# Optimization experiments

Hardware: AMD Instinct MI355X
Metric: run time of the kernel (lower is better)

Reference implementation:

```python
import jax, jax.numpy as jnp
import numpy as np

V, E, H = 50000, 128, 256  # vocab, embedding_size, hidden_size
S, B = 512, 64             # seq_len, batch (seq-first, torch LSTM default)


def setup_inputs() -> dict:
    key = jax.random.key(0)
    ks = jax.random.split(key, 10)
    u = 1.0 / np.sqrt(H)  # torch LSTM/Linear init bound

    def unif(k, sh):
        return jax.random.uniform(k, sh, jnp.float32, -u, u)

    emb = jax.random.normal(ks[0], (V, E), jnp.float32) * 0.02
    emb = emb.at[0].set(0.0)  # padding_idx=0

    inp = {
        "seq": jax.random.randint(ks[1], (S, B), 0, V),
        "emb": emb,
        # forward direction weights (gate order i,f,g,o like torch)
        "W_ih_f": unif(ks[2], (4 * H, E)),
        "W_hh_f": unif(ks[3], (4 * H, H)),
        "b_f": unif(ks[4], (4 * H,)),  # b_ih + b_hh fused (identical math)
        # reverse direction
        "W_ih_b": unif(ks[5], (4 * H, E)),
        "W_hh_b": unif(ks[6], (4 * H, H)),
        "b_b": unif(ks[7], (4 * H,)),
        # classification head over concatenated bi-directional features
        "W_out": unif(ks[8], (1, 2 * H)),
        "b_out": unif(ks[9], (1,)),
    }
    return inp


def _lstm_scan(xg, W_hh):
    """xg: [S,B,4H] precomputed input-gate projections; returns hidden seq [S,B,H]."""
    b = xg.shape[1]
    h0 = jnp.zeros((b, H), xg.dtype)
    c0 = jnp.zeros((b, H), xg.dtype)

    def step(carry, xg_t):
        h, c = carry
        gates = xg_t + h @ W_hh.T  # [B,4H]
        i, f, g, o = jnp.split(gates, 4, axis=-1)
        i = jax.nn.sigmoid(i)
        f = jax.nn.sigmoid(f)
        g = jnp.tanh(g)
        o = jax.nn.sigmoid(o)
        c = f * c + i * g
        h = o * jnp.tanh(c)
        return (h, c), h

    _, hs = jax.lax.scan(step, (h0, c0), xg)
    return hs


def reference(seq, emb, W_ih_f, W_hh_f, b_f, W_ih_b, W_hh_b, b_b, W_out, b_out):
    # embedding with padding_idx=0 (row 0 contributes zero)
    x = jnp.where((seq == 0)[..., None], 0.0, emb[seq])  # [S,B,E]

    xg_f = jnp.einsum("sbe,ge->sbg", x, W_ih_f) + b_f          # [S,B,4H]
    hs_f = _lstm_scan(xg_f, W_hh_f)                             # [S,B,H]

    xr = x[::-1]
    xg_b = jnp.einsum("sbe,ge->sbg", xr, W_ih_b) + b_b
    hs_b = _lstm_scan(xg_b, W_hh_b)[::-1]                       # [S,B,H]

    out = jnp.concatenate([hs_f, hs_b], axis=-1)                # [S,B,2H]
    last = out[-1]                                              # [B,2H]
    return jax.nn.sigmoid(last @ W_out.T + b_out)               # [B,1]
```

## Files before the change

### kernel.cpp

```cpp
#include <hip/hip_runtime.h>
#include <hip/hip_bf16.h>
#include <stdint.h>
#include <string.h>

#define S_LEN 512
#define NBATCH 64
#define EDIM 128
#define HDIM 256
#define GDIM 1024

#define WQ_SCALE 1024.0f
#define HQ_SCALE 127.0f
#define DEQ_SCALE (1.0f / 130048.0f)

typedef __attribute__((ext_vector_type(8))) short short8;
typedef __attribute__((ext_vector_type(4))) short short4v;
typedef __attribute__((ext_vector_type(4))) float float4v;
typedef __attribute__((ext_vector_type(4))) int int4v;

#define OFF_WHH8 0u
#define SZ_WHH8 (256u * 64u * 16u)
#define OFF_WIH (OFF_WHH8 + SZ_WHH8)
#define SZ_WIH (64u * 4u * 64u * 16u)
#define OFF_XG ((size_t)(OFF_WIH + SZ_WIH))
#define SZ_XG ((size_t)S_LEN * NBATCH * GDIM * 2)
#define OFF_HF (OFF_XG + SZ_XG)

__device__ __forceinline__ short f2bf(float f) {
    union { float f; unsigned u; } v;
    v.f = f;
    unsigned r = (v.u + 0x7fffu + ((v.u >> 16) & 1u)) >> 16;
    return (short)r;
}
__device__ __forceinline__ float bf2f(short s) {
    union { unsigned u; float f; } v;
    v.u = ((unsigned)(unsigned short)s) << 16;
    return v.f;
}
__device__ __forceinline__ float sigm(float x) {
    float e = __expf(-x);
    return __builtin_amdgcn_rcpf(1.0f + e);
}
__device__ __forceinline__ float tanh_(float x) {
    float e = __expf(2.0f * x);
    return 1.0f - 2.0f * __builtin_amdgcn_rcpf(e + 1.0f);
}

__global__ __launch_bounds__(256) void prep_frags(const float* __restrict__ src,
                                                  char* __restrict__ dst,
                                                  int K, int nchunks, int nfrags) {
    int id = blockIdx.x * blockDim.x + threadIdx.x;
    int lane = id & 63;
    int f = id >> 6;
    if (f >= nfrags) return;
    int tile = f / nchunks;
    int c = f - tile * nchunks;
    int row = tile * 16 + (lane & 15);
    int k0 = c * 32 + ((lane >> 4) * 8);
    const float* s = src + (size_t)row * K + k0;
    short8 pack;
#pragma unroll
    for (int j = 0; j < 8; ++j) pack[j] = f2bf(s[j]);
    *(short8*)(dst + ((size_t)f * 64 + lane) * 16) = pack;
}

__global__ __launch_bounds__(256) void prep_whh_i8(const float* __restrict__ src,
                                                   char* __restrict__ dst) {
    int id = blockIdx.x * blockDim.x + threadIdx.x;
    int lane = id & 63;
    int f = id >> 6;
    int tile = f >> 2, kc = f & 3;
    int row = tile * 16 + (lane & 15);
    int k0 = kc * 64 + ((lane >> 4) * 16);
    const float* s = src + (size_t)row * HDIM + k0;
    union { char b[16]; int4v v; } u;
#pragma unroll
    for (int b = 0; b < 16; ++b)
        u.b[b] = (char)(int)rintf(s[b] * WQ_SCALE);
    *(int4v*)(dst + ((size_t)f * 64 + lane) * 16) = u.v;
}

__global__ __launch_bounds__(256) void input_proj(const int* __restrict__ seq,
                                                  const float* __restrict__ emb,
                                                  const char* __restrict__ wih_frags,
                                                  const float* __restrict__ bias,
                                                  char* __restrict__ xg) {
    __shared__ __align__(16) short lx[4][16][136];
    int tid = threadIdx.x;
    int t0 = blockIdx.x * 4;
    int g = blockIdx.y;

    {
        int row = tid >> 2;
        int tt = row >> 4, m = row & 15;
        int k0 = (tid & 3) * 32;
        int v = seq[(t0 + tt) * NBATCH + g * 16 + m];
        const float* src = emb + (size_t)v * EDIM + k0;
        bool zero = (v == 0);
#pragma unroll
        for (int u = 0; u < 32; u += 4) {
            float4v f = *(const float4v*)(src + u);
            short4v p;
#pragma unroll
            for (int e = 0; e < 4; ++e) p[e] = zero ? (short)0 : f2bf(f[e]);
            *(short4v*)&lx[tt][m][k0 + u] = p;
        }
    }
    __syncthreads();

    int lane = tid & 63, w = tid >> 6;
    int ln = lane & 15, q = lane >> 4;

    short8 Bx[4][4];
#pragma unroll
    for (int tt = 0; tt < 4; ++tt)
#pragma unroll
        for (int c = 0; c < 4; ++c)
            Bx[tt][c] = *(const short8*)&lx[tt][ln][c * 32 + q * 8];

    for (int nt = 0; nt < 16; ++nt) {
        int tile = w * 16 + nt;
        short8 Aw[4];
#pragma unroll
        for (int c = 0; c < 4; ++c)
            Aw[c] = *(const short8*)(wih_frags + (((size_t)tile * 4 + c) * 64 + lane) * 16);
        float4v b4 = *(const float4v*)(bias + tile * 16 + q * 4);
#pragma unroll
        for (int tt = 0; tt < 4; ++tt) {
            float4v acc = b4;
#pragma unroll
            for (int c = 0; c < 4; ++c)
                acc = __builtin_amdgcn_mfma_f32_16x16x32_bf16(Aw[c], Bx[tt][c], acc, 0, 0, 0);
            short4v p;
#pragma unroll
            for (int r = 0; r < 4; ++r) p[r] = f2bf(acc[r]);
            size_t off = ((size_t)(t0 + tt) * NBATCH + g * 16 + ln) * GDIM + tile * 16 + q * 4;
            *(short4v*)(xg + off * 2) = p;
        }
    }
}

__global__ __launch_bounds__(1024, 4) void lstm_scan(const char* __restrict__ whh8,
                                                     const char* __restrict__ xg,
                                                     float* __restrict__ hf_out) {
    __shared__ __align__(16) char hls[2][16][272];
    __shared__ __align__(16) int scr[16][16 * 20];
    int tid = threadIdx.x;
    int lane = tid & 63, w = tid >> 6;
    int ln = lane & 15, q = lane >> 4;
    int bg = blockIdx.x;

    int4v Wfr[4][4];
#pragma unroll
    for (int blk = 0; blk < 4; ++blk) {
        int tile = 16 * blk + w;
#pragma unroll
        for (int kc = 0; kc < 4; ++kc)
            Wfr[blk][kc] = *(const int4v*)(whh8 + (((size_t)(tile * 4 + kc)) * 64 + lane) * 16);
    }

    {
        int* hp = (int*)&hls[0][0][0];
        for (int i = tid; i < (2 * 16 * 272) / 4; i += 1024) hp[i] = 0;
    }

    const char* hrd = &hls[0][0][0];
    char* hwr = &hls[1][0][0];
    int hoff_rd = ln * 272 + q * 16;

    int b = ln & 3;
    int rr = ln >> 2;
    int j = w * 16 + q * 4 + rr;
    int hoff_wr = b * 272 + j;
    int* swr = &scr[w][0] + (q * 4 + ln) * 20;
    const int* srd = &scr[w][0] + (q * 4 + b) * 20 + rr;

    float cst = 0.0f;

    const char* xgp = xg + (((size_t)(bg * 4 + b) * GDIM + j) * 2);
    const size_t tstep = (size_t)NBATCH * GDIM * 2;

    unsigned short xq[4];
#pragma unroll
    for (int blk = 0; blk < 4; ++blk)
        xq[blk] = *(const unsigned short*)(xgp + blk * 512);

    __syncthreads();

    for (int t = 0; t < S_LEN; ++t) {
        int4v Bh[4];
#pragma unroll
        for (int kc = 0; kc < 4; ++kc)
            Bh[kc] = *(const int4v*)(hrd + hoff_rd + kc * 64);

        float xgf[4];
#pragma unroll
        for (int blk = 0; blk < 4; ++blk) xgf[blk] = bf2f((short)xq[blk]);
        xgp += tstep;
        if (t != S_LEN - 1) {
#pragma unroll
            for (int blk = 0; blk < 4; ++blk)
                xq[blk] = *(const unsigned short*)(xgp + blk * 512);
        }

        int4v a[4];
#pragma unroll
        for (int blk = 0; blk < 4; ++blk) a[blk] = (int4v){0, 0, 0, 0};
#pragma unroll
        for (int kc = 0; kc < 4; ++kc)
#pragma unroll
            for (int blk = 0; blk < 4; ++blk)
                a[blk] = __builtin_amdgcn_mfma_i32_16x16x64_i8(Wfr[blk][kc], Bh[kc], a[blk], 0, 0, 0);

        if (ln < 4) {
#pragma unroll
            for (int blk = 0; blk < 4; ++blk)
                *(int4v*)(swr + blk * 4) = a[blk];
        }
        float gi = fmaf((float)srd[0], DEQ_SCALE, xgf[0]);
        float gf = fmaf((float)srd[4], DEQ_SCALE, xgf[1]);
        float gg = fmaf((float)srd[8], DEQ_SCALE, xgf[2]);
        float go = fmaf((float)srd[12], DEQ_SCALE, xgf[3]);

        float iv = sigm(gi);
        float fv = sigm(gf);
        float gv = tanh_(gg);
        float ov = sigm(go);
        float cv = fv * cst + iv * gv;
        cst = cv;
        float hv = ov * tanh_(cv);

        int hq = (int)rintf(hv * HQ_SCALE);
        hwr[hoff_wr] = (char)hq;

        if (t == S_LEN - 1)
            hf_out[((size_t)(bg * 4 + b)) * HDIM + j] = hv;

        const char* tr = hrd; hrd = hwr; hwr = (char*)tr;
        __syncthreads();
    }
}

__global__ __launch_bounds__(256) void tail_kernel(const int* __restrict__ seq,
                                                   const float* __restrict__ emb,
                                                   const float* __restrict__ wih_b,
                                                   const float* __restrict__ b_b,
                                                   const float* __restrict__ wout,
                                                   const float* __restrict__ b_out,
                                                   const float* __restrict__ hf,
                                                   float* __restrict__ out) {
    __shared__ float xs[EDIM];
    __shared__ float red[4];
    int b = blockIdx.x, tid = threadIdx.x;
    if (tid < EDIM) {
        int v = seq[(S_LEN - 1) * NBATCH + b];
        xs[tid] = (v == 0) ? 0.0f : emb[(size_t)v * EDIM + tid];
    }
    __syncthreads();

    int j = tid;
    float si = b_b[j], sg = b_b[2 * HDIM + j], so = b_b[3 * HDIM + j];
    const float* wi = wih_b + (size_t)j * EDIM;
    const float* wg = wih_b + (size_t)(2 * HDIM + j) * EDIM;
    const float* wo = wih_b + (size_t)(3 * HDIM + j) * EDIM;
#pragma unroll 8
    for (int k = 0; k < EDIM; k += 4) {
        float4v x4 = *(const float4v*)&xs[k];
        float4v a = *(const float4v*)(wi + k);
        float4v c = *(const float4v*)(wg + k);
        float4v d = *(const float4v*)(wo + k);
#pragma unroll
        for (int e = 0; e < 4; ++e) {
            si += a[e] * x4[e];
            sg += c[e] * x4[e];
            so += d[e] * x4[e];
        }
    }
    float cc = sigm(si) * tanh_(sg);
    float hb = sigm(so) * tanh_(cc);
    float partial = hf[(size_t)b * HDIM + j] * wout[j] + hb * wout[HDIM + j];

    float val = partial;
#pragma unroll
    for (int off = 32; off > 0; off >>= 1) val += __shfl_down(val, off, 64);
    int lane = tid & 63, wv = tid >> 6;
    if (lane == 0) red[wv] = val;
    __syncthreads();
    if (tid == 0) out[b] = sigm(red[0] + red[1] + red[2] + red[3] + b_out[0]);
}

extern "C" void kernel_launch(void* const* d_in, const int* in_sizes, int n_in,
                              void* d_out, int out_size, void* d_ws, size_t ws_size,
                              hipStream_t stream) {
    const int* seq = (const int*)d_in[0];
    const float* emb = (const float*)d_in[1];
    const float* Wih_f = (const float*)d_in[2];
    const float* Whh_f = (const float*)d_in[3];
    const float* b_f = (const float*)d_in[4];
    const float* Wih_b = (const float*)d_in[5];
    const float* b_b = (const float*)d_in[7];
    const float* Wout = (const float*)d_in[8];
    const float* b_out = (const float*)d_in[9];
    float* out = (float*)d_out;
    char* ws = (char*)d_ws;

    prep_whh_i8<<<dim3(64), 256, 0, stream>>>(Whh_f, ws + OFF_WHH8);
    prep_frags<<<dim3(64), 256, 0, stream>>>(Wih_f, ws + OFF_WIH, EDIM, 4, 64 * 4);
    input_proj<<<dim3(S_LEN / 4, 4), 256, 0, stream>>>(seq, emb, ws + OFF_WIH, b_f, ws + OFF_XG);
    lstm_scan<<<dim3(16), 1024, 0, stream>>>(ws + OFF_WHH8, ws + OFF_XG, (float*)(ws + OFF_HF));
    tail_kernel<<<dim3(NBATCH), 256, 0, stream>>>(seq, emb, Wih_b, b_b, Wout, b_out,
                                                  (const float*)(ws + OFF_HF), out);
}
```

Measured before the change: 697.6 us.

## Split LSTM scan into 32 blocks of 512 threads with prescaled exp2 gates

The recurrent scan now runs 32 workgroups of 8 waves, each handling 2 batch columns instead of 4, with each wave computing two tiles per gate. This spreads the serial scan across more CUs and shortens the per-step barrier. Gate pre-activations are prescaled in the input projection by -log2e or 2·log2e, and the dequant scale is folded into those constants. Sigmoid and tanh then become a single exp2 plus a fast reciprocal, with slight accuracy risk from bf16 storage of scaled values and approximate rcp.

```diff
diff --git a/kernel.cpp b/kernel.cpp
--- a/kernel.cpp
+++ b/kernel.cpp
@@ -11,7 +11,9 @@
 
 #define WQ_SCALE 1024.0f
 #define HQ_SCALE 127.0f
-#define DEQ_SCALE (1.0f / 130048.0f)
+#define LOG2E 1.4426950408889634f
+#define C_IFO (-1.1093545e-05f)
+#define C_G (2.2187090e-05f)
 
 typedef __attribute__((ext_vector_type(8))) short short8;
 typedef __attribute__((ext_vector_type(4))) short short4v;
@@ -120,6 +122,7 @@
 
     for (int nt = 0; nt < 16; ++nt) {
         int tile = w * 16 + nt;
+        float kg = ((tile >> 4) == 2) ? (2.0f * LOG2E) : (-LOG2E);
         short8 Aw[4];
 #pragma unroll
         for (int c = 0; c < 4; ++c)
@@ -133,60 +136,65 @@
                 acc = __builtin_amdgcn_mfma_f32_16x16x32_bf16(Aw[c], Bx[tt][c], acc, 0, 0, 0);
             short4v p;
 #pragma unroll
-            for (int r = 0; r < 4; ++r) p[r] = f2bf(acc[r]);
+            for (int r = 0; r < 4; ++r) p[r] = f2bf(acc[r] * kg);
             size_t off = ((size_t)(t0 + tt) * NBATCH + g * 16 + ln) * GDIM + tile * 16 + q * 4;
             *(short4v*)(xg + off * 2) = p;
         }
     }
 }
 
-__global__ __launch_bounds__(1024, 4) void lstm_scan(const char* __restrict__ whh8,
-                                                     const char* __restrict__ xg,
-                                                     float* __restrict__ hf_out) {
+__global__ __launch_bounds__(512, 2) void lstm_scan(const char* __restrict__ whh8,
+                                                    const char* __restrict__ xg,
+                                                    float* __restrict__ hf_out) {
     __shared__ __align__(16) char hls[2][16][272];
-    __shared__ __align__(16) int scr[16][16 * 20];
+    __shared__ __align__(16) int scr[8][256];
     int tid = threadIdx.x;
     int lane = tid & 63, w = tid >> 6;
     int ln = lane & 15, q = lane >> 4;
     int bg = blockIdx.x;
 
-    int4v Wfr[4][4];
-#pragma unroll
-    for (int blk = 0; blk < 4; ++blk) {
-        int tile = 16 * blk + w;
-#pragma unroll
-        for (int kc = 0; kc < 4; ++kc)
-            Wfr[blk][kc] = *(const int4v*)(whh8 + (((size_t)(tile * 4 + kc)) * 64 + lane) * 16);
-    }
+    int4v Wfr[4][2][4];
+#pragma unroll
+    for (int g = 0; g < 4; ++g)
+#pragma unroll
+        for (int p = 0; p < 2; ++p) {
+            int tile = g * 16 + (w * 2 + p);
+#pragma unroll
+            for (int kc = 0; kc < 4; ++kc)
+                Wfr[g][p][kc] = *(const int4v*)(whh8 + (((size_t)(tile * 4 + kc)) * 64 + lane) * 16);
+        }
 
     {
         int* hp = (int*)&hls[0][0][0];
-        for (int i = tid; i < (2 * 16 * 272) / 4; i += 1024) hp[i] = 0;
+        for (int i = tid; i < (2 * 16 * 272) / 4; i += 512) hp[i] = 0;
     }
 
     const char* hrd = &hls[0][0][0];
     char* hwr = &hls[1][0][0];
     int hoff_rd = ln * 272 + q * 16;
 
-    int b = ln & 3;
-    int rr = ln >> 2;
-    int j = w * 16 + q * 4 + rr;
+    int b = ln & 1;
+    int rr = (ln >> 1) & 3;
+    int p = ln >> 3;
+    int j = (w * 2 + p) * 16 + q * 4 + rr;
     int hoff_wr = b * 272 + j;
-    int* swr = &scr[w][0] + (q * 4 + ln) * 20;
-    const int* srd = &scr[w][0] + (q * 4 + b) * 20 + rr;
+
+    int* swr = &scr[w][0];
+    const int* srd = &scr[w][0] + (q * 16 + p * 8 + b * 4 + rr);
 
     float cst = 0.0f;
 
-    const char* xgp = xg + (((size_t)(bg * 4 + b) * GDIM + j) * 2);
+    const char* xgp = xg + (((size_t)(bg * 2 + b) * GDIM + j) * 2);
     const size_t tstep = (size_t)NBATCH * GDIM * 2;
 
     unsigned short xq[4];
 #pragma unroll
-    for (int blk = 0; blk < 4; ++blk)
-        xq[blk] = *(const unsigned short*)(xgp + blk * 512);
+    for (int g = 0; g < 4; ++g)
+        xq[g] = *(const unsigned short*)(xgp + g * 512);
 
     __syncthreads();
 
+    const int4v z4 = {0, 0, 0, 0};
     for (int t = 0; t < S_LEN; ++t) {
         int4v Bh[4];
 #pragma unroll
@@ -195,46 +203,54 @@
 
         float xgf[4];
 #pragma unroll
-        for (int blk = 0; blk < 4; ++blk) xgf[blk] = bf2f((short)xq[blk]);
+        for (int g = 0; g < 4; ++g) xgf[g] = bf2f((short)xq[g]);
         xgp += tstep;
         if (t != S_LEN - 1) {
 #pragma unroll
-            for (int blk = 0; blk < 4; ++blk)
-                xq[blk] = *(const unsigned short*)(xgp + blk * 512);
-        }
-
-        int4v a[4];
-#pragma unroll
-        for (int blk = 0; blk < 4; ++blk) a[blk] = (int4v){0, 0, 0, 0};
-#pragma unroll
-        for (int kc = 0; kc < 4; ++kc)
-#pragma unroll
-            for (int blk = 0; blk < 4; ++blk)
-                a[blk] = __builtin_amdgcn_mfma_i32_16x16x64_i8(Wfr[blk][kc], Bh[kc], a[blk], 0, 0, 0);
-
-        if (ln < 4) {
-#pragma unroll
-            for (int blk = 0; blk < 4; ++blk)
-                *(int4v*)(swr + blk * 4) = a[blk];
-        }
-        float gi = fmaf((float)srd[0], DEQ_SCALE, xgf[0]);
-        float gf = fmaf((float)srd[4], DEQ_SCALE, xgf[1]);
-        float gg = fmaf((float)srd[8], DEQ_SCALE, xgf[2]);
-        float go = fmaf((float)srd[12], DEQ_SCALE, xgf[3]);
-
-        float iv = sigm(gi);
-        float fv = sigm(gf);
-        float gv = tanh_(gg);
-        float ov = sigm(go);
-        float cv = fv * cst + iv * gv;
+            for (int g = 0; g < 4; ++g)
+                xq[g] = *(const unsigned short*)(xgp + g * 512);
+        }
+
+        int4v a[4][2];
+#pragma unroll
+        for (int g = 0; g < 4; ++g)
+#pragma unroll
+            for (int pp = 0; pp < 2; ++pp)
+                a[g][pp] = __builtin_amdgcn_mfma_i32_16x16x64_i8(Wfr[g][pp][0], Bh[0], z4, 0, 0, 0);
+#pragma unroll
+        for (int kc = 1; kc < 4; ++kc)
+#pragma unroll
+            for (int g = 0; g < 4; ++g)
+#pragma unroll
+                for (int pp = 0; pp < 2; ++pp)
+                    a[g][pp] = __builtin_amdgcn_mfma_i32_16x16x64_i8(Wfr[g][pp][kc], Bh[kc], a[g][pp], 0, 0, 0);
+
+        if (ln < 2) {
+#pragma unroll
+            for (int g = 0; g < 4; ++g)
+#pragma unroll
+                for (int pp = 0; pp < 2; ++pp)
+                    *(int4v*)(swr + g * 64 + q * 16 + pp * 8 + ln * 4) = a[g][pp];
+        }
+        float s0 = fmaf((float)srd[0], C_IFO, xgf[0]);
+        float s1 = fmaf((float)srd[64], C_IFO, xgf[1]);
+        float s2 = fmaf((float)srd[128], C_G, xgf[2]);
+        float s3 = fmaf((float)srd[192], C_IFO, xgf[3]);
+
+        float iv = __builtin_amdgcn_rcpf(1.0f + exp2f(s0));
+        float fv = __builtin_amdgcn_rcpf(1.0f + exp2f(s1));
+        float gv = fmaf(-2.0f, __builtin_amdgcn_rcpf(1.0f + exp2f(s2)), 1.0f);
+        float ov = __builtin_amdgcn_rcpf(1.0f + exp2f(s3));
+        float cv = fmaf(fv, cst, iv * gv);
         cst = cv;
-        float hv = ov * tanh_(cv);
+        float tc = fmaf(-2.0f, __builtin_amdgcn_rcpf(1.0f + exp2f(cv * (2.0f * LOG2E))), 1.0f);
+        float hv = ov * tc;
 
         int hq = (int)rintf(hv * HQ_SCALE);
         hwr[hoff_wr] = (char)hq;
 
         if (t == S_LEN - 1)
-            hf_out[((size_t)(bg * 4 + b)) * HDIM + j] = hv;
+            hf_out[((size_t)(bg * 2 + b)) * HDIM + j] = hv;
 
         const char* tr = hrd; hrd = hwr; hwr = (char*)tr;
         __syncthreads();
@@ -307,7 +323,7 @@
     prep_whh_i8<<<dim3(64), 256, 0, stream>>>(Whh_f, ws + OFF_WHH8);
     prep_frags<<<dim3(64), 256, 0, stream>>>(Wih_f, ws + OFF_WIH, EDIM, 4, 64 * 4);
     input_proj<<<dim3(S_LEN / 4, 4), 256, 0, stream>>>(seq, emb, ws + OFF_WIH, b_f, ws + OFF_XG);
-    lstm_scan<<<dim3(16), 1024, 0, stream>>>(ws + OFF_WHH8, ws + OFF_XG, (float*)(ws + OFF_HF));
+    lstm_scan<<<dim3(32), 512, 0, stream>>>(ws + OFF_WHH8, ws + OFF_XG, (float*)(ws + OFF_HF));
     tail_kernel<<<dim3(NBATCH), 256, 0, stream>>>(seq, emb, Wih_b, b_b, Wout, b_out,
                                                   (const float*)(ws + OFF_HF), out);
 }
```

New measurement: 723.0 us. 3.6% more time.
